# Kernel tuning notes

Measured on AMD Instinct MI355X. Metric: run time of the kernel, lower is better.

The kernel has to match this reference:

```python
import jax, jax.numpy as jnp
import numpy as np

N_NODES = 50000


def setup_inputs() -> dict:
    key = jax.random.key(0)
    k1, k2, k3, k4, k5, k6 = jax.random.split(key, 6)
    N, T, F_IN, F_OUT, E = N_NODES, 4, 64, 64, 800000
    node_features = jax.random.normal(k1, (N, T, F_IN), dtype=jnp.float32)
    edge_weights = jax.random.uniform(k2, (T, E), dtype=jnp.float32)
    src = jax.random.randint(k3, (E,), 0, N, dtype=jnp.int32)
    dst = jax.random.randint(k4, (E,), 0, N, dtype=jnp.int32)
    weight = jax.random.normal(k5, (F_OUT, F_IN), dtype=jnp.float32) / np.sqrt(F_IN)
    bias = jax.random.normal(k6, (F_OUT,), dtype=jnp.float32) * 0.01
    return {"node_features": node_features, "edge_weights": edge_weights,
            "src": src, "dst": dst, "weight": weight, "bias": bias}


def reference(node_features, edge_weights, src, dst, weight, bias):
    # edge_weights: (T, E) -> per-edge weights (E, T)
    ew = edge_weights.T  # (E, T)
    # gather source node features: (E, T, F); multiply by per-edge/timestep scalar
    msg = ew[:, :, None] * node_features[src]  # (E, T, F)
    # scatter-sum into destination nodes: (N, T, F)
    h = jax.ops.segment_sum(msg, dst, num_segments=N_NODES)
    # final linear: (N, T, F_out)
    out = jnp.einsum('ntf,of->nto', h, weight) + bias
    return out
```

## Files before the change

### kernel.cpp

```cpp
#include <hip/hip_runtime.h>


#define F_DIM 64
#define TF 256

typedef __attribute__((ext_vector_type(8))) short bf16x8;
typedef __attribute__((ext_vector_type(4))) float f32x4;
union frag_u { bf16x8 v; unsigned short s[8]; };

__device__ __forceinline__ unsigned short f2bf(float x) {
  unsigned u = __float_as_uint(x);
  return (unsigned short)((u + 0x7FFF + ((u >> 16) & 1)) >> 16);
}
__device__ __forceinline__ float bf2f(unsigned short b) {
  return __uint_as_float(((unsigned)b) << 16);
}

__global__ __launch_bounds__(1024) void scanA_kernel(
    const int* __restrict__ cnt, int* __restrict__ off, int* __restrict__ bsum, int N) {
  __shared__ int wsum[16];
  int tid = threadIdx.x;
  int i = blockIdx.x * 1024 + tid;
  int v = (i < N) ? cnt[i] : 0;
  int lane = tid & 63;
  int incl = v;
  #pragma unroll
  for (int s = 1; s < 64; s <<= 1) {
    int t = __shfl_up(incl, s, 64);
    if (lane >= s) incl += t;
  }
  int w = tid >> 6;
  if (lane == 63) wsum[w] = incl;
  __syncthreads();
  if (w == 0) {
    int x = (lane < 16) ? wsum[lane] : 0;
    #pragma unroll
    for (int s = 1; s < 16; s <<= 1) {
      int t = __shfl_up(x, s, 64);
      if (lane >= s) x += t;
    }
    if (lane < 16) wsum[lane] = x;
  }
  __syncthreads();
  int wpre = (w == 0) ? 0 : wsum[w - 1];
  if (i < N) off[i] = wpre + incl - v;
  if (tid == 1023) bsum[blockIdx.x] = wpre + incl;
}

__global__ __launch_bounds__(64) void scanB_kernel(int* __restrict__ bsum, int nb) {
  int lane = threadIdx.x;
  int v = (lane < nb) ? bsum[lane] : 0;
  int incl = v;
  #pragma unroll
  for (int s = 1; s < 64; s <<= 1) {
    int t = __shfl_up(incl, s, 64);
    if (lane >= s) incl += t;
  }
  if (lane < nb) bsum[lane] = incl - v;
}

__global__ __launch_bounds__(256) void fill_kernel(
    const int* __restrict__ dst, const int* __restrict__ src,
    const float* __restrict__ ew, const int* __restrict__ off,
    const int* __restrict__ bsum, int* __restrict__ cnt,
    uint4* __restrict__ rec, int E) {
  int e = blockIdx.x * 256 + threadIdx.x;
  if (e < E) {
    int d = dst[e];
    int pos = off[d] + bsum[d >> 10] + atomicSub(&cnt[d], 1) - 1;
    unsigned w0 = f2bf(ew[e]),         w1 = f2bf(ew[E + e]);
    unsigned w2 = f2bf(ew[2 * E + e]), w3 = f2bf(ew[3 * E + e]);
    uint4 r;
    r.x = (unsigned)src[e];
    r.y = (w1 << 16) | w0;
    r.z = (w3 << 16) | w2;
    r.w = 0;
    rec[pos] = r;
  }
}

__global__ __launch_bounds__(256) void transform_hist_kernel(
    const float4* __restrict__ nf4, const float* __restrict__ W,
    unsigned short* __restrict__ nfb, int nrows,
    const int* __restrict__ dst, int* __restrict__ cnt, int E) {
  int lane = threadIdx.x & 63;
  int l15 = lane & 15, lg = lane >> 4;
  int wid = (blockIdx.x * 256 + threadIdx.x) >> 6;
  int nw = (gridDim.x * 256) >> 6;

  frag_u a[4][2];
  #pragma unroll
  for (int ot = 0; ot < 4; ++ot) {
    #pragma unroll
    for (int kh = 0; kh < 2; ++kh) {
      const float* wp = W + (ot * 16 + l15) * 64 + kh * 32 + lg * 8;
      float4 v0 = *reinterpret_cast<const float4*>(wp);
      float4 v1 = *reinterpret_cast<const float4*>(wp + 4);
      a[ot][kh].s[0] = f2bf(v0.x); a[ot][kh].s[1] = f2bf(v0.y);
      a[ot][kh].s[2] = f2bf(v0.z); a[ot][kh].s[3] = f2bf(v0.w);
      a[ot][kh].s[4] = f2bf(v1.x); a[ot][kh].s[5] = f2bf(v1.y);
      a[ot][kh].s[6] = f2bf(v1.z); a[ot][kh].s[7] = f2bf(v1.w);
    }
  }

  int ntiles = (nrows + 15) >> 4;
  for (int tile = wid; tile < ntiles; tile += nw) {
    int r = tile * 16 + l15;
    int rc = min(r, nrows - 1);
    const float4* bp = nf4 + (size_t)rc * 16 + lg * 2;
    float4 v0 = bp[0], v1 = bp[1];
    float4 v2 = bp[8], v3 = bp[9];
    frag_u b0, b1;
    b0.s[0] = f2bf(v0.x); b0.s[1] = f2bf(v0.y);
    b0.s[2] = f2bf(v0.z); b0.s[3] = f2bf(v0.w);
    b0.s[4] = f2bf(v1.x); b0.s[5] = f2bf(v1.y);
    b0.s[6] = f2bf(v1.z); b0.s[7] = f2bf(v1.w);
    b1.s[0] = f2bf(v2.x); b1.s[1] = f2bf(v2.y);
    b1.s[2] = f2bf(v2.z); b1.s[3] = f2bf(v2.w);
    b1.s[4] = f2bf(v3.x); b1.s[5] = f2bf(v3.y);
    b1.s[6] = f2bf(v3.z); b1.s[7] = f2bf(v3.w);

    f32x4 acc[4];
    #pragma unroll
    for (int ot = 0; ot < 4; ++ot) {
      f32x4 z = {0.f, 0.f, 0.f, 0.f};
      acc[ot] = __builtin_amdgcn_mfma_f32_16x16x32_bf16(a[ot][0].v, b0.v, z, 0, 0, 0);
      acc[ot] = __builtin_amdgcn_mfma_f32_16x16x32_bf16(a[ot][1].v, b1.v, acc[ot], 0, 0, 0);
    }
    if (r < nrows) {
      #pragma unroll
      for (int ot = 0; ot < 4; ++ot) {
        ushort4 u = make_ushort4(f2bf(acc[ot][0]), f2bf(acc[ot][1]),
                                 f2bf(acc[ot][2]), f2bf(acc[ot][3]));
        *reinterpret_cast<ushort4*>(
            &nfb[(size_t)r * F_DIM + ot * 16 + lg * 4]) = u;
      }
    }
  }

  int gtid = blockIdx.x * 256 + threadIdx.x;
  int gsz = gridDim.x * 256;
  for (int e = gtid; e < E; e += gsz) atomicAdd(&cnt[dst[e]], 1);
}

__global__ __launch_bounds__(256) void gather_bf16_kernel(
    const ushort4* __restrict__ nfb, const uint4* __restrict__ rec,
    const int* __restrict__ off, const int* __restrict__ bsum,
    const float4* __restrict__ bias4, float4* __restrict__ out4, int N, int E) {
  int idx = blockIdx.x * 256 + threadIdx.x;
  int n = idx >> 6;
  if (n >= N) return;
  n = __builtin_amdgcn_readfirstlane(n);
  int r = idx & 63, t = r >> 4, q = r & 15;
  int wsel = t >> 1;
  int wshift = (t & 1) << 4;
  int beg = off[n] + bsum[n >> 10];
  int end = (n + 1 < N) ? off[n + 1] + bsum[(n + 1) >> 10] : E;
  beg = __builtin_amdgcn_readfirstlane(beg);
  end = __builtin_amdgcn_readfirstlane(end);

  float4 acc = make_float4(0.f, 0.f, 0.f, 0.f);
  int p = beg;
  for (; p + 4 <= end; p += 4) {
    uint4 r0 = rec[p], r1 = rec[p + 1], r2 = rec[p + 2], r3 = rec[p + 3];
    float w0 = __uint_as_float(((wsel ? r0.z : r0.y) >> wshift) << 16);
    float w1 = __uint_as_float(((wsel ? r1.z : r1.y) >> wshift) << 16);
    float w2 = __uint_as_float(((wsel ? r2.z : r2.y) >> wshift) << 16);
    float w3 = __uint_as_float(((wsel ? r3.z : r3.y) >> wshift) << 16);
    ushort4 v0 = nfb[(size_t)r0.x * 64 + t * 16 + q];
    ushort4 v1 = nfb[(size_t)r1.x * 64 + t * 16 + q];
    ushort4 v2 = nfb[(size_t)r2.x * 64 + t * 16 + q];
    ushort4 v3 = nfb[(size_t)r3.x * 64 + t * 16 + q];
    acc.x += w0 * bf2f(v0.x) + w1 * bf2f(v1.x) + w2 * bf2f(v2.x) + w3 * bf2f(v3.x);
    acc.y += w0 * bf2f(v0.y) + w1 * bf2f(v1.y) + w2 * bf2f(v2.y) + w3 * bf2f(v3.y);
    acc.z += w0 * bf2f(v0.z) + w1 * bf2f(v1.z) + w2 * bf2f(v2.z) + w3 * bf2f(v3.z);
    acc.w += w0 * bf2f(v0.w) + w1 * bf2f(v1.w) + w2 * bf2f(v2.w) + w3 * bf2f(v3.w);
  }
  for (; p < end; ++p) {
    uint4 rr = rec[p];
    float w = __uint_as_float(((wsel ? rr.z : rr.y) >> wshift) << 16);
    ushort4 v = nfb[(size_t)rr.x * 64 + t * 16 + q];
    acc.x += w * bf2f(v.x); acc.y += w * bf2f(v.y);
    acc.z += w * bf2f(v.z); acc.w += w * bf2f(v.w);
  }
  float4 b = bias4[q];
  float4 res = make_float4(acc.x + b.x, acc.y + b.y, acc.z + b.z, acc.w + b.w);
  out4[(size_t)n * 64 + t * 16 + q] = res;
}

__global__ __launch_bounds__(256) void hist_kernel(
    const int* __restrict__ dst, int* __restrict__ cnt, int E) {
  int e = blockIdx.x * 256 + threadIdx.x;
  if (e < E) atomicAdd(&cnt[dst[e]], 1);
}

__global__ __launch_bounds__(256) void gather_f32_kernel(
    const float4* __restrict__ nf4, const uint4* __restrict__ rec,
    const int* __restrict__ off, const int* __restrict__ bsum,
    float4* __restrict__ h4, int N, int E) {
  int idx = blockIdx.x * 256 + threadIdx.x;
  int n = idx >> 6;
  if (n >= N) return;
  int r = idx & 63, t = r >> 4, q = r & 15;
  int wsel = t >> 1;
  int wshift = (t & 1) << 4;
  int beg = off[n] + bsum[n >> 10];
  int end = (n + 1 < N) ? off[n + 1] + bsum[(n + 1) >> 10] : E;
  float4 acc = make_float4(0.f, 0.f, 0.f, 0.f);
  for (int p = beg; p < end; ++p) {
    uint4 rr = rec[p];
    float w = __uint_as_float(((wsel ? rr.z : rr.y) >> wshift) << 16);
    float4 v = nf4[(size_t)rr.x * 64 + t * 16 + q];
    acc.x += w * v.x; acc.y += w * v.y; acc.z += w * v.z; acc.w += w * v.w;
  }
  h4[(size_t)n * 64 + t * 16 + q] = acc;
}

__global__ __launch_bounds__(256) void linear_kernel(
    float* __restrict__ h, const float* __restrict__ W,
    const float* __restrict__ bias, int nrows) {
  __shared__ float Wt[64 * 65];
  __shared__ float rows[4][64];
  int tid = threadIdx.x;
  for (int i = tid; i < 4096; i += 256) Wt[(i & 63) * 65 + (i >> 6)] = W[i];
  int rr = tid >> 6, o = tid & 63;
  float b = bias[o];
  int rbase = blockIdx.x * 32;
  for (int r0 = 0; r0 < 32; r0 += 4) {
    int row = rbase + r0 + rr;
    __syncthreads();
    if (row < nrows) rows[rr][o] = h[(size_t)row * F_DIM + o];
    __syncthreads();
    if (row < nrows) {
      float acc = b;
      #pragma unroll
      for (int f = 0; f < 64; ++f) acc += rows[rr][f] * Wt[f * 65 + o];
      h[(size_t)row * F_DIM + o] = acc;
    }
  }
}

extern "C" void kernel_launch(void* const* d_in, const int* in_sizes, int n_in,
                              void* d_out, int out_size, void* d_ws, size_t ws_size,
                              hipStream_t stream) {
  const float* nf   = (const float*)d_in[0];
  const float* ew   = (const float*)d_in[1];
  const int*   src  = (const int*)d_in[2];
  const int*   dst  = (const int*)d_in[3];
  const float* W    = (const float*)d_in[4];
  const float* bias = (const float*)d_in[5];
  float* out = (float*)d_out;

  int E = in_sizes[2];
  int N = out_size / TF;
  int nrows = out_size / F_DIM;
  int nfelems = nrows * F_DIM;

  char* wsb = (char*)d_ws;
  int* cnt  = (int*)wsb;
  int* off  = cnt + N;
  int* bsum = off + (N + 1);
  size_t ofs = ((size_t)(2 * N + 1 + 64) * 4 + 15) & ~(size_t)15;
  uint4* rec = (uint4*)(wsb + ofs);           ofs += (size_t)E * 16;
  ofs = (ofs + 511) & ~(size_t)511;
  unsigned short* nfb = (unsigned short*)(wsb + ofs);
  size_t need_bf16 = ofs + (size_t)nfelems * 2;
  bool use_bf16 = ws_size >= need_bf16;

  (void)hipMemsetAsync(cnt, 0, (size_t)N * sizeof(int), stream);

  int eblk = (E + 255) / 256;
  int sblk = (N + 1023) / 1024;

  if (use_bf16) {
    transform_hist_kernel<<<1024, 256, 0, stream>>>(
        (const float4*)nf, W, nfb, nrows, dst, cnt, E);
    scanA_kernel<<<sblk, 1024, 0, stream>>>(cnt, off, bsum, N);
    scanB_kernel<<<1, 64, 0, stream>>>(bsum, sblk);
    fill_kernel<<<eblk, 256, 0, stream>>>(dst, src, ew, off, bsum, cnt, rec, E);
    gather_bf16_kernel<<<(N * 64 + 255) / 256, 256, 0, stream>>>(
        (const ushort4*)nfb, rec, off, bsum, (const float4*)bias,
        (float4*)out, N, E);
  } else {
    hist_kernel<<<eblk, 256, 0, stream>>>(dst, cnt, E);
    scanA_kernel<<<sblk, 1024, 0, stream>>>(cnt, off, bsum, N);
    scanB_kernel<<<1, 64, 0, stream>>>(bsum, sblk);
    fill_kernel<<<eblk, 256, 0, stream>>>(dst, src, ew, off, bsum, cnt, rec, E);
    gather_f32_kernel<<<(N * 64 + 255) / 256, 256, 0, stream>>>(
        (const float4*)nf, rec, off, bsum, (float4*)out, N, E);
    linear_kernel<<<(nrows + 31) / 32, 256, 0, stream>>>(out, W, bias, nrows);
  }
}
```

Before: 160.2 us.

## Fuse CSR fill with bf16 feature transform; run histogram standalone first

```diff
diff --git a/kernel.cpp b/kernel.cpp
--- a/kernel.cpp
+++ b/kernel.cpp
@@ -14,6 +14,12 @@
 }
 __device__ __forceinline__ float bf2f(unsigned short b) {
   return __uint_as_float(((unsigned)b) << 16);
+}
+
+__global__ __launch_bounds__(256) void hist_kernel(
+    const int* __restrict__ dst, int* __restrict__ cnt, int E) {
+  int e = blockIdx.x * 256 + threadIdx.x;
+  if (e < E) atomicAdd(&cnt[dst[e]], 1);
 }
 
 __global__ __launch_bounds__(1024) void scanA_kernel(
@@ -57,6 +63,148 @@
     if (lane >= s) incl += t;
   }
   if (lane < nb) bsum[lane] = incl - v;
+}
+
+__global__ __launch_bounds__(256) void fill_transform_kernel(
+    const int* __restrict__ dst, const int* __restrict__ src,
+    const float* __restrict__ ew, const int* __restrict__ off,
+    const int* __restrict__ bsum, int* __restrict__ cnt,
+    uint4* __restrict__ rec, int E, int fillBlocks,
+    const float4* __restrict__ nf4, const float* __restrict__ W,
+    unsigned short* __restrict__ nfb, int nrows) {
+  int tid = threadIdx.x;
+  if ((int)blockIdx.x < fillBlocks) {
+    int stride = fillBlocks * 256;
+    for (int e = blockIdx.x * 256 + tid; e < E; e += stride) {
+      int d = dst[e];
+      int pos = off[d] + bsum[d >> 10] + atomicSub(&cnt[d], 1) - 1;
+      unsigned w0 = f2bf(ew[e]),         w1 = f2bf(ew[E + e]);
+      unsigned w2 = f2bf(ew[2 * E + e]), w3 = f2bf(ew[3 * E + e]);
+      uint4 r;
+      r.x = (unsigned)src[e];
+      r.y = (w1 << 16) | w0;
+      r.z = (w3 << 16) | w2;
+      r.w = 0;
+      rec[pos] = r;
+    }
+    return;
+  }
+
+  int lane = tid & 63;
+  int l15 = lane & 15, lg = lane >> 4;
+  int wid = (((int)blockIdx.x - fillBlocks) * 256 + tid) >> 6;
+  int nw = ((gridDim.x - fillBlocks) * 256) >> 6;
+
+  frag_u a[4][2];
+  #pragma unroll
+  for (int ot = 0; ot < 4; ++ot) {
+    #pragma unroll
+    for (int kh = 0; kh < 2; ++kh) {
+      const float* wp = W + (ot * 16 + l15) * 64 + kh * 32 + lg * 8;
+      float4 v0 = *reinterpret_cast<const float4*>(wp);
+      float4 v1 = *reinterpret_cast<const float4*>(wp + 4);
+      a[ot][kh].s[0] = f2bf(v0.x); a[ot][kh].s[1] = f2bf(v0.y);
+      a[ot][kh].s[2] = f2bf(v0.z); a[ot][kh].s[3] = f2bf(v0.w);
+      a[ot][kh].s[4] = f2bf(v1.x); a[ot][kh].s[5] = f2bf(v1.y);
+      a[ot][kh].s[6] = f2bf(v1.z); a[ot][kh].s[7] = f2bf(v1.w);
+    }
+  }
+
+  int ntiles = (nrows + 15) >> 4;
+  for (int tile = wid; tile < ntiles; tile += nw) {
+    int r = tile * 16 + l15;
+    int rc = min(r, nrows - 1);
+    const float4* bp = nf4 + (size_t)rc * 16 + lg * 2;
+    float4 v0 = bp[0], v1 = bp[1];
+    float4 v2 = bp[8], v3 = bp[9];
+    frag_u b0, b1;
+    b0.s[0] = f2bf(v0.x); b0.s[1] = f2bf(v0.y);
+    b0.s[2] = f2bf(v0.z); b0.s[3] = f2bf(v0.w);
+    b0.s[4] = f2bf(v1.x); b0.s[5] = f2bf(v1.y);
+    b0.s[6] = f2bf(v1.z); b0.s[7] = f2bf(v1.w);
+    b1.s[0] = f2bf(v2.x); b1.s[1] = f2bf(v2.y);
+    b1.s[2] = f2bf(v2.z); b1.s[3] = f2bf(v2.w);
+    b1.s[4] = f2bf(v3.x); b1.s[5] = f2bf(v3.y);
+    b1.s[6] = f2bf(v3.z); b1.s[7] = f2bf(v3.w);
+
+    f32x4 acc[4];
+    #pragma unroll
+    for (int ot = 0; ot < 4; ++ot) {
+      f32x4 z = {0.f, 0.f, 0.f, 0.f};
+      acc[ot] = __builtin_amdgcn_mfma_f32_16x16x32_bf16(a[ot][0].v, b0.v, z, 0, 0, 0);
+      acc[ot] = __builtin_amdgcn_mfma_f32_16x16x32_bf16(a[ot][1].v, b1.v, acc[ot], 0, 0, 0);
+    }
+    if (r < nrows) {
+      #pragma unroll
+      for (int ot = 0; ot < 4; ++ot) {
+        ushort4 u = make_ushort4(f2bf(acc[ot][0]), f2bf(acc[ot][1]),
+                                 f2bf(acc[ot][2]), f2bf(acc[ot][3]));
+        *reinterpret_cast<ushort4*>(
+            &nfb[(size_t)r * F_DIM + ot * 16 + lg * 4]) = u;
+      }
+    }
+  }
+}
+
+__global__ __launch_bounds__(256) void gather_bf16_kernel(
+    const ushort4* __restrict__ nfb, const uint4* __restrict__ rec,
+    const int* __restrict__ off, const int* __restrict__ bsum,
+    const float4* __restrict__ bias4, float4* __restrict__ out4, int N, int E) {
+  int idx = blockIdx.x * 256 + threadIdx.x;
+  int n = idx >> 6;
+  if (n >= N) return;
+  n = __builtin_amdgcn_readfirstlane(n);
+  int r = idx & 63, t = r >> 4, q = r & 15;
+  int wsel = t >> 1;
+  int wshift = (t & 1) << 4;
+  int beg = off[n] + bsum[n >> 10];
+  int end = (n + 1 < N) ? off[n + 1] + bsum[(n + 1) >> 10] : E;
+  beg = __builtin_amdgcn_readfirstlane(beg);
+  end = __builtin_amdgcn_readfirstlane(end);
+
+  float4 acc = make_float4(0.f, 0.f, 0.f, 0.f);
+  int p = beg;
+  for (; p + 8 <= end; p += 8) {
+    uint4 rr[8];
+    #pragma unroll
+    for (int j = 0; j < 8; ++j) rr[j] = rec[p + j];
+    float w[8];
+    ushort4 v[8];
+    #pragma unroll
+    for (int j = 0; j < 8; ++j) {
+      w[j] = __uint_as_float(((wsel ? rr[j].z : rr[j].y) >> wshift) << 16);
+      v[j] = nfb[(size_t)rr[j].x * 64 + t * 16 + q];
+    }
+    #pragma unroll
+    for (int j = 0; j < 8; ++j) {
+      acc.x += w[j] * bf2f(v[j].x);
+      acc.y += w[j] * bf2f(v[j].y);
+      acc.z += w[j] * bf2f(v[j].z);
+      acc.w += w[j] * bf2f(v[j].w);
+    }
+  }
+  for (; p + 4 <= end; p += 4) {
+    uint4 rr[4];
+    #pragma unroll
+    for (int j = 0; j < 4; ++j) rr[j] = rec[p + j];
+    #pragma unroll
+    for (int j = 0; j < 4; ++j) {
+      float w = __uint_as_float(((wsel ? rr[j].z : rr[j].y) >> wshift) << 16);
+      ushort4 v = nfb[(size_t)rr[j].x * 64 + t * 16 + q];
+      acc.x += w * bf2f(v.x); acc.y += w * bf2f(v.y);
+      acc.z += w * bf2f(v.z); acc.w += w * bf2f(v.w);
+    }
+  }
+  for (; p < end; ++p) {
+    uint4 rr = rec[p];
+    float w = __uint_as_float(((wsel ? rr.z : rr.y) >> wshift) << 16);
+    ushort4 v = nfb[(size_t)rr.x * 64 + t * 16 + q];
+    acc.x += w * bf2f(v.x); acc.y += w * bf2f(v.y);
+    acc.z += w * bf2f(v.z); acc.w += w * bf2f(v.w);
+  }
+  float4 b = bias4[q];
+  float4 res = make_float4(acc.x + b.x, acc.y + b.y, acc.z + b.z, acc.w + b.w);
+  out4[(size_t)n * 64 + t * 16 + q] = res;
 }
 
 __global__ __launch_bounds__(256) void fill_kernel(
@@ -77,121 +225,6 @@
     r.w = 0;
     rec[pos] = r;
   }
-}
-
-__global__ __launch_bounds__(256) void transform_hist_kernel(
-    const float4* __restrict__ nf4, const float* __restrict__ W,
-    unsigned short* __restrict__ nfb, int nrows,
-    const int* __restrict__ dst, int* __restrict__ cnt, int E) {
-  int lane = threadIdx.x & 63;
-  int l15 = lane & 15, lg = lane >> 4;
-  int wid = (blockIdx.x * 256 + threadIdx.x) >> 6;
-  int nw = (gridDim.x * 256) >> 6;
-
-  frag_u a[4][2];
-  #pragma unroll
-  for (int ot = 0; ot < 4; ++ot) {
-    #pragma unroll
-    for (int kh = 0; kh < 2; ++kh) {
-      const float* wp = W + (ot * 16 + l15) * 64 + kh * 32 + lg * 8;
-      float4 v0 = *reinterpret_cast<const float4*>(wp);
-      float4 v1 = *reinterpret_cast<const float4*>(wp + 4);
-      a[ot][kh].s[0] = f2bf(v0.x); a[ot][kh].s[1] = f2bf(v0.y);
-      a[ot][kh].s[2] = f2bf(v0.z); a[ot][kh].s[3] = f2bf(v0.w);
-      a[ot][kh].s[4] = f2bf(v1.x); a[ot][kh].s[5] = f2bf(v1.y);
-      a[ot][kh].s[6] = f2bf(v1.z); a[ot][kh].s[7] = f2bf(v1.w);
-    }
-  }
-
-  int ntiles = (nrows + 15) >> 4;
-  for (int tile = wid; tile < ntiles; tile += nw) {
-    int r = tile * 16 + l15;
-    int rc = min(r, nrows - 1);
-    const float4* bp = nf4 + (size_t)rc * 16 + lg * 2;
-    float4 v0 = bp[0], v1 = bp[1];
-    float4 v2 = bp[8], v3 = bp[9];
-    frag_u b0, b1;
-    b0.s[0] = f2bf(v0.x); b0.s[1] = f2bf(v0.y);
-    b0.s[2] = f2bf(v0.z); b0.s[3] = f2bf(v0.w);
-    b0.s[4] = f2bf(v1.x); b0.s[5] = f2bf(v1.y);
-    b0.s[6] = f2bf(v1.z); b0.s[7] = f2bf(v1.w);
-    b1.s[0] = f2bf(v2.x); b1.s[1] = f2bf(v2.y);
-    b1.s[2] = f2bf(v2.z); b1.s[3] = f2bf(v2.w);
-    b1.s[4] = f2bf(v3.x); b1.s[5] = f2bf(v3.y);
-    b1.s[6] = f2bf(v3.z); b1.s[7] = f2bf(v3.w);
-
-    f32x4 acc[4];
-    #pragma unroll
-    for (int ot = 0; ot < 4; ++ot) {
-      f32x4 z = {0.f, 0.f, 0.f, 0.f};
-      acc[ot] = __builtin_amdgcn_mfma_f32_16x16x32_bf16(a[ot][0].v, b0.v, z, 0, 0, 0);
-      acc[ot] = __builtin_amdgcn_mfma_f32_16x16x32_bf16(a[ot][1].v, b1.v, acc[ot], 0, 0, 0);
-    }
-    if (r < nrows) {
-      #pragma unroll
-      for (int ot = 0; ot < 4; ++ot) {
-        ushort4 u = make_ushort4(f2bf(acc[ot][0]), f2bf(acc[ot][1]),
-                                 f2bf(acc[ot][2]), f2bf(acc[ot][3]));
-        *reinterpret_cast<ushort4*>(
-            &nfb[(size_t)r * F_DIM + ot * 16 + lg * 4]) = u;
-      }
-    }
-  }
-
-  int gtid = blockIdx.x * 256 + threadIdx.x;
-  int gsz = gridDim.x * 256;
-  for (int e = gtid; e < E; e += gsz) atomicAdd(&cnt[dst[e]], 1);
-}
-
-__global__ __launch_bounds__(256) void gather_bf16_kernel(
-    const ushort4* __restrict__ nfb, const uint4* __restrict__ rec,
-    const int* __restrict__ off, const int* __restrict__ bsum,
-    const float4* __restrict__ bias4, float4* __restrict__ out4, int N, int E) {
-  int idx = blockIdx.x * 256 + threadIdx.x;
-  int n = idx >> 6;
-  if (n >= N) return;
-  n = __builtin_amdgcn_readfirstlane(n);
-  int r = idx & 63, t = r >> 4, q = r & 15;
-  int wsel = t >> 1;
-  int wshift = (t & 1) << 4;
-  int beg = off[n] + bsum[n >> 10];
-  int end = (n + 1 < N) ? off[n + 1] + bsum[(n + 1) >> 10] : E;
-  beg = __builtin_amdgcn_readfirstlane(beg);
-  end = __builtin_amdgcn_readfirstlane(end);
-
-  float4 acc = make_float4(0.f, 0.f, 0.f, 0.f);
-  int p = beg;
-  for (; p + 4 <= end; p += 4) {
-    uint4 r0 = rec[p], r1 = rec[p + 1], r2 = rec[p + 2], r3 = rec[p + 3];
-    float w0 = __uint_as_float(((wsel ? r0.z : r0.y) >> wshift) << 16);
-    float w1 = __uint_as_float(((wsel ? r1.z : r1.y) >> wshift) << 16);
-    float w2 = __uint_as_float(((wsel ? r2.z : r2.y) >> wshift) << 16);
-    float w3 = __uint_as_float(((wsel ? r3.z : r3.y) >> wshift) << 16);
-    ushort4 v0 = nfb[(size_t)r0.x * 64 + t * 16 + q];
-    ushort4 v1 = nfb[(size_t)r1.x * 64 + t * 16 + q];
-    ushort4 v2 = nfb[(size_t)r2.x * 64 + t * 16 + q];
-    ushort4 v3 = nfb[(size_t)r3.x * 64 + t * 16 + q];
-    acc.x += w0 * bf2f(v0.x) + w1 * bf2f(v1.x) + w2 * bf2f(v2.x) + w3 * bf2f(v3.x);
-    acc.y += w0 * bf2f(v0.y) + w1 * bf2f(v1.y) + w2 * bf2f(v2.y) + w3 * bf2f(v3.y);
-    acc.z += w0 * bf2f(v0.z) + w1 * bf2f(v1.z) + w2 * bf2f(v2.z) + w3 * bf2f(v3.z);
-    acc.w += w0 * bf2f(v0.w) + w1 * bf2f(v1.w) + w2 * bf2f(v2.w) + w3 * bf2f(v3.w);
-  }
-  for (; p < end; ++p) {
-    uint4 rr = rec[p];
-    float w = __uint_as_float(((wsel ? rr.z : rr.y) >> wshift) << 16);
-    ushort4 v = nfb[(size_t)rr.x * 64 + t * 16 + q];
-    acc.x += w * bf2f(v.x); acc.y += w * bf2f(v.y);
-    acc.z += w * bf2f(v.z); acc.w += w * bf2f(v.w);
-  }
-  float4 b = bias4[q];
-  float4 res = make_float4(acc.x + b.x, acc.y + b.y, acc.z + b.z, acc.w + b.w);
-  out4[(size_t)n * 64 + t * 16 + q] = res;
-}
-
-__global__ __launch_bounds__(256) void hist_kernel(
-    const int* __restrict__ dst, int* __restrict__ cnt, int E) {
-  int e = blockIdx.x * 256 + threadIdx.x;
-  if (e < E) atomicAdd(&cnt[dst[e]], 1);
 }
 
 __global__ __launch_bounds__(256) void gather_f32_kernel(
@@ -272,19 +305,20 @@
   int eblk = (E + 255) / 256;
   int sblk = (N + 1023) / 1024;
 
+  hist_kernel<<<eblk, 256, 0, stream>>>(dst, cnt, E);
+  scanA_kernel<<<sblk, 1024, 0, stream>>>(cnt, off, bsum, N);
+  scanB_kernel<<<1, 64, 0, stream>>>(bsum, sblk);
+
   if (use_bf16) {
-    transform_hist_kernel<<<1024, 256, 0, stream>>>(
-        (const float4*)nf, W, nfb, nrows, dst, cnt, E);
-    scanA_kernel<<<sblk, 1024, 0, stream>>>(cnt, off, bsum, N);
-    scanB_kernel<<<1, 64, 0, stream>>>(bsum, sblk);
-    fill_kernel<<<eblk, 256, 0, stream>>>(dst, src, ew, off, bsum, cnt, rec, E);
+    int fillBlocks = 1024;
+    int transformBlocks = 1024;
+    fill_transform_kernel<<<fillBlocks + transformBlocks, 256, 0, stream>>>(
+        dst, src, ew, off, bsum, cnt, rec, E, fillBlocks,
+        (const float4*)nf, W, nfb, nrows);
     gather_bf16_kernel<<<(N * 64 + 255) / 256, 256, 0, stream>>>(
         (const ushort4*)nfb, rec, off, bsum, (const float4*)bias,
         (float4*)out, N, E);
   } else {
-    hist_kernel<<<eblk, 256, 0, stream>>>(dst, cnt, E);
-    scanA_kernel<<<sblk, 1024, 0, stream>>>(cnt, off, bsum, N);
-    scanB_kernel<<<1, 64, 0, stream>>>(bsum, sblk);
     fill_kernel<<<eblk, 256, 0, stream>>>(dst, src, ew, off, bsum, cnt, rec, E);
     gather_f32_kernel<<<(N * 64 + 255) / 256, 256, 0, stream>>>(
         (const float4*)nf, rec, off, bsum, (float4*)out, N, E);
```

After: 163.0 us. About the same (+1.7%).
